# Optimization experiments

Measured on AMD Instinct MI355X. Metric: run time of the kernel, lower is better.

## Reference

```python
import jax, jax.numpy as jnp
import numpy as np

D_MODEL = 1024
N_HEADS = 16
HEAD_DIM = D_MODEL // N_HEADS
SCALE = HEAD_DIM ** -0.5
MASK_FILL = -10000.0


def setup_inputs() -> dict:
    key = jax.random.key(0)
    ks = jax.random.split(key, 12)
    B, L, D = 2, 2048, D_MODEL
    inv = 1.0 / np.sqrt(D)
    inp = {
        "query": jax.random.normal(ks[0], (B, L, D), jnp.float32),
        "key": jax.random.normal(ks[1], (B, L, D), jnp.float32),
        "value": jax.random.normal(ks[2], (B, L, D), jnp.float32),
        "Wq": jax.random.normal(ks[3], (D, D), jnp.float32) * inv,
        "bq": jnp.zeros((D,), jnp.float32),
        "Wk": jax.random.normal(ks[4], (D, D), jnp.float32) * inv,
        "bk": jnp.zeros((D,), jnp.float32),
        "Wv": jax.random.normal(ks[5], (D, D), jnp.float32) * inv,
        "bv": jnp.zeros((D,), jnp.float32),
        "Wo": jax.random.normal(ks[6], (D, D), jnp.float32) * inv,
        "bo": jnp.zeros((D,), jnp.float32),
        "valid_mask": jax.random.randint(ks[7], (B, L), 0, 2).astype(jnp.bool_),
    }
    return inp


def reference(query, key, value, Wq, bq, Wk, bk, Wv, bv, Wo, bo, valid_mask):
    B, Lq, D = query.shape
    Lk = key.shape[1]
    H, HD = N_HEADS, HEAD_DIM
    # torch.nn.Linear: y = x @ W.T + b
    Q = (query @ Wq.T + bq).reshape(B, Lq, H, HD).transpose(0, 2, 1, 3)  # [B,H,Lq,HD]
    K = (key @ Wk.T + bk).reshape(B, Lk, H, HD).transpose(0, 2, 1, 3)    # [B,H,Lk,HD]
    V = (value @ Wv.T + bv).reshape(B, Lk, H, HD).transpose(0, 2, 1, 3)  # [B,H,Lk,HD]
    scores = jnp.einsum("bhqd,bhkd->bhqk", Q, K) * SCALE
    scores = jnp.where(valid_mask[:, None, None, :], scores, MASK_FILL)
    weights = jax.nn.softmax(scores, axis=-1)  # dropout is identity at inference
    out = jnp.einsum("bhqk,bhkd->bhqd", weights, V)
    out = out.transpose(0, 2, 1, 3).reshape(B, Lq, D)
    out = out @ Wo.T + bo
    # zero rows of fully-invalid batches
    gate = jnp.any(valid_mask, axis=1).astype(out.dtype)[:, None, None]
    return out * gate
```

## Files before the change

### kernel.cpp

```cpp
#include <hip/hip_runtime.h>
#include <hip/hip_bf16.h>

typedef __hip_bfloat16 bf16;
typedef __attribute__((ext_vector_type(8))) short s8v;
typedef __attribute__((ext_vector_type(4))) float f4v;

#define LOG2E 1.44269504088896340736f
#define CSCALE (0.125f * LOG2E)
#define MASK_B2 (-14426.950408889634f)

#define BB 2
#define LL 2048
#define DD 1024
#define HH 16
#define HD 64
#define MTOT 4096
#define PER_T 4194304

struct alignas(8) B4 { bf16 v[4]; };

__device__ __forceinline__ void async_cp16(const bf16* g, bf16* l) {
    __builtin_amdgcn_global_load_lds(
        (const __attribute__((address_space(1))) void*)g,
        (__attribute__((address_space(3))) void*)l, 16, 0, 0);
}

struct CvtArgs {
    const float* src[7];
    bf16* dst[7];
    int n[7];
};

__global__ __launch_bounds__(256) void cvt_kernel(CvtArgs args) {
    const int which = blockIdx.y;
    const float* __restrict__ src = args.src[which];
    bf16* __restrict__ dst = args.dst[which];
    const int n4 = args.n[which] >> 2;
    const int stride = gridDim.x * 256;
    for (int i = blockIdx.x * 256 + threadIdx.x; i < n4; i += stride) {
        const float4 f = ((const float4*)src)[i];
        B4 o;
        o.v[0] = __float2bfloat16(f.x);
        o.v[1] = __float2bfloat16(f.y);
        o.v[2] = __float2bfloat16(f.z);
        o.v[3] = __float2bfloat16(f.w);
        ((B4*)dst)[i] = o;
    }
}

struct QkvArgs {
    const bf16* A[3];
    const bf16* W[3];
    const float* bias[3];
    bf16* out[3];
};

template <int SWAP>
__device__ __forceinline__ void gemm_body(const bf16* __restrict__ A,
                                          const bf16* __restrict__ W,
                                          const float* __restrict__ bias,
                                          bf16* __restrict__ out_bf,
                                          char* smem) {
    bf16* sA = (bf16*)smem;
    bf16* sB = (bf16*)(smem + 128 * 64 * 2);
    bf16* sE = (bf16*)smem;

    const int lane = threadIdx.x & 63;
    const int w = threadIdx.x >> 6;
    const int lr = lane & 15;
    const int quad = lane >> 4;
    const int wr = w >> 1, wc = w & 1;
    const int rbase = blockIdx.x * 128;
    const int cbase = blockIdx.y * 128;
    const int dma_r = lane >> 3;
    const int dma_cc = ((lane & 7) ^ dma_r) * 8;

    f4v acc[4][4] = {};
    for (int kt = 0; kt < DD / 64; kt++) {
        const int k0 = kt * 64;
        __syncthreads();
#pragma unroll
        for (int t = 0; t < 4; t++) {
            const int g = w * 4 + t;
            async_cp16(A + (size_t)(rbase + g * 8 + dma_r) * DD + k0 + dma_cc,
                       &sA[g * 512]);
            async_cp16(W + (size_t)(cbase + g * 8 + dma_r) * DD + k0 + dma_cc,
                       &sB[g * 512]);
        }
        __syncthreads();
#pragma unroll
        for (int s = 0; s < 2; s++) {
            s8v a[4], b[4];
#pragma unroll
            for (int i = 0; i < 4; i++) {
                const int row = wr * 64 + i * 16 + lr;
                a[i] = *(const s8v*)&sA[row * 64 + (((s * 4 + quad) ^ (row & 7)) * 8)];
            }
#pragma unroll
            for (int j = 0; j < 4; j++) {
                const int row = wc * 64 + j * 16 + lr;
                b[j] = *(const s8v*)&sB[row * 64 + (((s * 4 + quad) ^ (row & 7)) * 8)];
            }
#pragma unroll
            for (int i = 0; i < 4; i++)
#pragma unroll
                for (int j = 0; j < 4; j++)
                    acc[i][j] = SWAP
                        ? __builtin_amdgcn_mfma_f32_16x16x32_bf16(b[j], a[i], acc[i][j], 0, 0, 0)
                        : __builtin_amdgcn_mfma_f32_16x16x32_bf16(a[i], b[j], acc[i][j], 0, 0, 0);
        }
    }
    __syncthreads();

    if (SWAP) {
#pragma unroll
        for (int j = 0; j < 4; j++) {
            const int n_loc = wc * 64 + j * 16 + quad * 4;
            const f4v bv = *(const f4v*)&bias[cbase + n_loc];
#pragma unroll
            for (int i = 0; i < 4; i++) {
                const int m_loc = wr * 64 + i * 16 + lr;
                B4 pk;
                pk.v[0] = __float2bfloat16(acc[i][j][0] + bv[0]);
                pk.v[1] = __float2bfloat16(acc[i][j][1] + bv[1]);
                pk.v[2] = __float2bfloat16(acc[i][j][2] + bv[2]);
                pk.v[3] = __float2bfloat16(acc[i][j][3] + bv[3]);
                *(B4*)&sE[m_loc * 136 + n_loc] = pk;
            }
        }
        __syncthreads();
        const int tid = threadIdx.x;
        const int mr_ = tid >> 4;
        const int n0 = (tid & 15) * 8;
#pragma unroll
        for (int ro = 0; ro < 8; ro++) {
            const int m_loc = ro * 16 + mr_;
            const s8v vv = *(const s8v*)&sE[m_loc * 136 + n0];
            const int m = rbase + m_loc;
            const int n = cbase + n0;
            const int b_ = m >> 11, l = m & (LL - 1);
            const int h = n >> 6, hd = n & 63;
            *(s8v*)&out_bf[(((size_t)(b_ * HH + h)) * LL + l) * HD + hd] = vv;
        }
    } else {
#pragma unroll
        for (int j = 0; j < 4; j++) {
            const int n_loc = wc * 64 + j * 16 + lr;
            const float bv = bias[cbase + n_loc];
#pragma unroll
            for (int i = 0; i < 4; i++) {
                const int m0 = wr * 64 + i * 16 + quad * 4;
                B4 pk;
                pk.v[0] = __float2bfloat16(acc[i][j][0] + bv);
                pk.v[1] = __float2bfloat16(acc[i][j][1] + bv);
                pk.v[2] = __float2bfloat16(acc[i][j][2] + bv);
                pk.v[3] = __float2bfloat16(acc[i][j][3] + bv);
                *(B4*)&sE[n_loc * 136 + m0] = pk;
            }
        }
        __syncthreads();
        const int tid = threadIdx.x;
#pragma unroll
        for (int ro = 0; ro < 8; ro++) {
            const int n_loc = ro * 16 + (tid >> 4);
            const int m0 = (tid & 15) * 8;
            const s8v vv = *(const s8v*)&sE[n_loc * 136 + m0];
            const int n = cbase + n_loc;
            const int m = rbase + m0;
            const int b_ = m >> 11, l = m & (LL - 1);
            const int h = n >> 6, hd = n & 63;
            *(s8v*)&out_bf[(((size_t)(b_ * HH + h)) * HD + hd) * LL + l] = vv;
        }
    }
}

__global__ __launch_bounds__(256) void gemm128(QkvArgs qa) {
    __shared__ __align__(16) char smem[128 * 136 * 2];
    const int which = blockIdx.z;
    if (which != 2)
        gemm_body<1>(qa.A[which], qa.W[which], qa.bias[which], qa.out[which], smem);
    else
        gemm_body<0>(qa.A[2], qa.W[2], qa.bias[2], qa.out[2], smem);
}

__global__ __launch_bounds__(256) void oproj64(const bf16* __restrict__ A,
                                               const bf16* __restrict__ W,
                                               const float* __restrict__ bias,
                                               float* __restrict__ out_f,
                                               const int* __restrict__ mask) {
    __shared__ bf16 sA[64 * 64];
    __shared__ bf16 sB[128 * 64];
    __shared__ int sgate;

    const int lane = threadIdx.x & 63;
    const int w = threadIdx.x >> 6;
    const int lr = lane & 15;
    const int quad = lane >> 4;
    const int wr = w >> 1, wc = w & 1;
    const int rbase = blockIdx.x * 64;
    const int cbase = blockIdx.y * 128;
    const int dma_r = lane >> 3;
    const int dma_cc = ((lane & 7) ^ dma_r) * 8;

    if (threadIdx.x == 0) sgate = 0;
    __syncthreads();
    const int b_g = rbase >> 11;
    int any = 0;
    for (int i = threadIdx.x; i < LL; i += 256) any |= mask[b_g * LL + i];
    if (any) sgate = 1;

    f4v acc[2][4] = {};
    for (int kt = 0; kt < DD / 64; kt++) {
        const int k0 = kt * 64;
        __syncthreads();
#pragma unroll
        for (int t = 0; t < 2; t++) {
            const int g = w * 2 + t;
            async_cp16(A + (size_t)(rbase + g * 8 + dma_r) * DD + k0 + dma_cc,
                       &sA[g * 512]);
        }
#pragma unroll
        for (int t = 0; t < 4; t++) {
            const int g = w * 4 + t;
            async_cp16(W + (size_t)(cbase + g * 8 + dma_r) * DD + k0 + dma_cc,
                       &sB[g * 512]);
        }
        __syncthreads();
#pragma unroll
        for (int s = 0; s < 2; s++) {
            s8v a[2], b[4];
#pragma unroll
            for (int i = 0; i < 2; i++) {
                const int row = wr * 32 + i * 16 + lr;
                a[i] = *(const s8v*)&sA[row * 64 + (((s * 4 + quad) ^ (row & 7)) * 8)];
            }
#pragma unroll
            for (int j = 0; j < 4; j++) {
                const int row = wc * 64 + j * 16 + lr;
                b[j] = *(const s8v*)&sB[row * 64 + (((s * 4 + quad) ^ (row & 7)) * 8)];
            }
#pragma unroll
            for (int i = 0; i < 2; i++)
#pragma unroll
                for (int j = 0; j < 4; j++)
                    acc[i][j] = __builtin_amdgcn_mfma_f32_16x16x32_bf16(b[j], a[i], acc[i][j], 0, 0, 0);
        }
    }

    const float gatef = sgate ? 1.0f : 0.0f;
#pragma unroll
    for (int j = 0; j < 4; j++) {
        const int n = cbase + wc * 64 + j * 16 + quad * 4;
        const f4v bv = *(const f4v*)&bias[n];
#pragma unroll
        for (int i = 0; i < 2; i++) {
            const int m = rbase + wr * 32 + i * 16 + lr;
            float4 o;
            o.x = (acc[i][j][0] + bv[0]) * gatef;
            o.y = (acc[i][j][1] + bv[1]) * gatef;
            o.z = (acc[i][j][2] + bv[2]) * gatef;
            o.w = (acc[i][j][3] + bv[3]) * gatef;
            *(float4*)&out_f[(size_t)m * DD + n] = o;
        }
    }
}

__global__ __launch_bounds__(512) void attn_kernel(const bf16* __restrict__ Q,
                                                   const bf16* __restrict__ K,
                                                   const bf16* __restrict__ Vt,
                                                   const int* __restrict__ mask,
                                                   bf16* __restrict__ Aout) {
    __shared__ bf16 sK[2][64 * 64];
    __shared__ bf16 sV[2][64 * 64];
    __shared__ float sBias[LL];

    const int lane = threadIdx.x & 63;
    const int w = threadIdx.x >> 6;
    const int lr = lane & 15;
    const int quad = lane >> 4;

    const int bid = blockIdx.x;
    const int qb = bid & 15;
    const int h = (bid >> 4) & 15;
    const int b = bid >> 8;

    const size_t head_off = ((size_t)(b * HH + h)) * LL * HD;
    const bf16* Qh = Q + head_off;
    const bf16* Kh = K + head_off;
    const bf16* Vh = Vt + head_off;
    const int q0 = qb * 128 + w * 16;

    const int dma_r = lane >> 3;
    const int dma_cv = ((lane & 7) ^ dma_r) * 8;
    const int dma_ck = ((lane & 7) ^ ((dma_r & 3) | ((w & 1) << 2))) * 8;

    {
        const int* mb = mask + b * LL;
        for (int i = threadIdx.x; i < LL; i += 512)
            sBias[i] = mb[i] ? 0.0f : MASK_B2;
        async_cp16(Kh + (size_t)(w * 8 + dma_r) * HD + dma_ck, &sK[0][w * 512]);
        async_cp16(Vh + (size_t)(w * 8 + dma_r) * LL + dma_cv, &sV[0][w * 512]);
    }
    __syncthreads();

    const s8v aq0 = *(const s8v*)(Qh + (size_t)(q0 + lr) * HD + quad * 8);
    const s8v aq1 = *(const s8v*)(Qh + (size_t)(q0 + lr) * HD + 32 + quad * 8);

    f4v O[4] = {};
    float lacc = 0.0f;

    const int swk = (lr & 3) | (((lr >> 2) & 1) << 2);
    const int swv = lr & 7;
    const int krow0 = 8 * (lr >> 2) + (lr & 3);

    for (int kt = 0; kt < LL / 64; kt++) {
        const int kbase = kt * 64;
        const bf16* kb = &sK[kt & 1][0];
        const bf16* vb = &sV[kt & 1][0];

        if (kt < LL / 64 - 1) {
            const int nb = (kt + 1) & 1;
            async_cp16(Kh + (size_t)(kbase + 64 + w * 8 + dma_r) * HD + dma_ck,
                       &sK[nb][w * 512]);
            async_cp16(Vh + (size_t)(w * 8 + dma_r) * LL + kbase + 64 + dma_cv,
                       &sV[nb][w * 512]);
        }

        f4v T[4];
        __builtin_amdgcn_s_setprio(1);
#pragma unroll
        for (int j = 0; j < 4; j++) {
            const int row = krow0 + 32 * (j >> 1) + 4 * (j & 1);
            const s8v kb0 = *(const s8v*)&kb[row * 64 + ((quad ^ swk) * 8)];
            const s8v kb1 = *(const s8v*)&kb[row * 64 + (((quad + 4) ^ swk) * 8)];
            f4v t = {};
            t = __builtin_amdgcn_mfma_f32_16x16x32_bf16(kb0, aq0, t, 0, 0, 0);
            T[j] = __builtin_amdgcn_mfma_f32_16x16x32_bf16(kb1, aq1, t, 0, 0, 0);
        }
        __builtin_amdgcn_s_setprio(0);

        s8v v0[4], v1[4];
#pragma unroll
        for (int dt = 0; dt < 4; dt++) {
            const int vrow = dt * 16 + lr;
            v0[dt] = *(const s8v*)&vb[vrow * 64 + ((quad ^ swv) * 8)];
            v1[dt] = *(const s8v*)&vb[vrow * 64 + (((quad + 4) ^ swv) * 8)];
        }

        union { s8v v; bf16 e[8]; } p0, p1;
#pragma unroll
        for (int j = 0; j < 4; j++) {
            const f4v bj = *(const f4v*)&sBias[kbase + 32 * (j >> 1) + 8 * quad + 4 * (j & 1)];
#pragma unroll
            for (int r = 0; r < 4; r++) {
                const float e = exp2f(T[j][r] * CSCALE + bj[r]);
                T[j][r] = e;
                lacc += e;
            }
        }
#pragma unroll
        for (int r = 0; r < 4; r++) {
            p0.e[r]     = __float2bfloat16(T[0][r]);
            p0.e[r + 4] = __float2bfloat16(T[1][r]);
            p1.e[r]     = __float2bfloat16(T[2][r]);
            p1.e[r + 4] = __float2bfloat16(T[3][r]);
        }

        __builtin_amdgcn_s_setprio(1);
#pragma unroll
        for (int dt = 0; dt < 4; dt++) {
            O[dt] = __builtin_amdgcn_mfma_f32_16x16x32_bf16(v0[dt], p0.v, O[dt], 0, 0, 0);
            O[dt] = __builtin_amdgcn_mfma_f32_16x16x32_bf16(v1[dt], p1.v, O[dt], 0, 0, 0);
        }
        __builtin_amdgcn_s_setprio(0);

        __syncthreads();
    }

    float lt = lacc;
    lt += __shfl_xor(lt, 16);
    lt += __shfl_xor(lt, 32);
    const float linv = (lt > 0.0f) ? (1.0f / lt) : 0.0f;

#pragma unroll
    for (int dt = 0; dt < 4; dt++) {
        B4 o;
#pragma unroll
        for (int r = 0; r < 4; r++) o.v[r] = __float2bfloat16(O[dt][r] * linv);
        *(B4*)&Aout[((size_t)(b * LL + q0 + lr)) * DD + h * HD + dt * 16 + quad * 4] = o;
    }
}

extern "C" void kernel_launch(void* const* d_in, const int* in_sizes, int n_in,
                              void* d_out, int out_size, void* d_ws, size_t ws_size,
                              hipStream_t stream) {
    const float* query = (const float*)d_in[0];
    const float* key   = (const float*)d_in[1];
    const float* value = (const float*)d_in[2];
    const float* Wq = (const float*)d_in[3];
    const float* bq = (const float*)d_in[4];
    const float* Wk = (const float*)d_in[5];
    const float* bk = (const float*)d_in[6];
    const float* Wv = (const float*)d_in[7];
    const float* bv = (const float*)d_in[8];
    const float* Wo = (const float*)d_in[9];
    const float* bo = (const float*)d_in[10];
    const int* mask = (const int*)d_in[11];

    bf16* base = (bf16*)d_ws;
    bf16* qx = base;
    bf16* kx = qx + PER_T;
    bf16* vx = kx + PER_T;
    bf16* wq = vx + PER_T;
    bf16* wk = wq + DD * DD;
    bf16* wv = wk + DD * DD;
    bf16* wo = wv + DD * DD;
    bf16* Qs = wo + DD * DD;
    bf16* Ks = Qs + PER_T;
    bf16* Vst = Ks + PER_T;
    bf16* aws = Vst + PER_T;

    CvtArgs ca;
    ca.src[0] = query; ca.dst[0] = qx; ca.n[0] = PER_T;
    ca.src[1] = key;   ca.dst[1] = kx; ca.n[1] = PER_T;
    ca.src[2] = value; ca.dst[2] = vx; ca.n[2] = PER_T;
    ca.src[3] = Wq;    ca.dst[3] = wq; ca.n[3] = DD * DD;
    ca.src[4] = Wk;    ca.dst[4] = wk; ca.n[4] = DD * DD;
    ca.src[5] = Wv;    ca.dst[5] = wv; ca.n[5] = DD * DD;
    ca.src[6] = Wo;    ca.dst[6] = wo; ca.n[6] = DD * DD;
    cvt_kernel<<<dim3(1024, 7), 256, 0, stream>>>(ca);

    QkvArgs qa;
    qa.A[0] = qx; qa.W[0] = wq; qa.bias[0] = bq; qa.out[0] = Qs;
    qa.A[1] = kx; qa.W[1] = wk; qa.bias[1] = bk; qa.out[1] = Ks;
    qa.A[2] = vx; qa.W[2] = wv; qa.bias[2] = bv; qa.out[2] = Vst;

    gemm128<<<dim3(MTOT / 128, DD / 128, 3), 256, 0, stream>>>(qa);

    attn_kernel<<<BB * HH * (LL / 128), 512, 0, stream>>>(Qs, Ks, Vst, mask, aws);

    oproj64<<<dim3(MTOT / 64, DD / 128), 256, 0, stream>>>(
        aws, wo, bo, (float*)d_out, mask);
}
```

Measured before the change: 239.4 us.

## Fuse fp32-to-bf16 activation conversion into QKV GEMM operand loads

The separate conversion pass over query/key/value is removed. The QKV GEMM now streams fp32 activations straight into LDS with an XOR swizzle and converts them to bf16 at fragment-load time. This drops a full read/write pass of roughly 48MB of activations plus the bf16 re-read. The cost is double-size A tiles in LDS, which may cut occupancy, extra conversion ALU work in the inner loop, and re-conversion of each A tile by every column block.

```diff
diff --git a/kernel.cpp b/kernel.cpp
--- a/kernel.cpp
+++ b/kernel.cpp
@@ -19,16 +19,16 @@
 
 struct alignas(8) B4 { bf16 v[4]; };
 
-__device__ __forceinline__ void async_cp16(const bf16* g, bf16* l) {
+__device__ __forceinline__ void async_cp16(const void* g, void* l) {
     __builtin_amdgcn_global_load_lds(
         (const __attribute__((address_space(1))) void*)g,
         (__attribute__((address_space(3))) void*)l, 16, 0, 0);
 }
 
 struct CvtArgs {
-    const float* src[7];
-    bf16* dst[7];
-    int n[7];
+    const float* src[4];
+    bf16* dst[4];
+    int n[4];
 };
 
 __global__ __launch_bounds__(256) void cvt_kernel(CvtArgs args) {
@@ -49,20 +49,20 @@
 }
 
 struct QkvArgs {
-    const bf16* A[3];
+    const float* A[3];
     const bf16* W[3];
     const float* bias[3];
     bf16* out[3];
 };
 
 template <int SWAP>
-__device__ __forceinline__ void gemm_body(const bf16* __restrict__ A,
+__device__ __forceinline__ void gemm_body(const float* __restrict__ Af,
                                           const bf16* __restrict__ W,
                                           const float* __restrict__ bias,
                                           bf16* __restrict__ out_bf,
                                           char* smem) {
-    bf16* sA = (bf16*)smem;
-    bf16* sB = (bf16*)(smem + 128 * 64 * 2);
+    float* sAf = (float*)smem;
+    bf16* sB = (bf16*)(smem + 128 * 64 * 4);
     bf16* sE = (bf16*)smem;
 
     const int lane = threadIdx.x & 63;
@@ -82,10 +82,17 @@
 #pragma unroll
         for (int t = 0; t < 4; t++) {
             const int g = w * 4 + t;
-            async_cp16(A + (size_t)(rbase + g * 8 + dma_r) * DD + k0 + dma_cc,
-                       &sA[g * 512]);
             async_cp16(W + (size_t)(cbase + g * 8 + dma_r) * DD + k0 + dma_cc,
                        &sB[g * 512]);
+#pragma unroll
+            for (int c = 0; c < 2; c++) {
+                const int row_in_g = c * 4 + (lane >> 4);
+                const int swz = (8 * (g & 1) + row_in_g) & 15;
+                const int src_chunk = (lane & 15) ^ swz;
+                async_cp16(Af + (size_t)(rbase + g * 8 + row_in_g) * DD + k0 +
+                               src_chunk * 4,
+                           &sAf[g * 512 + c * 256]);
+            }
         }
         __syncthreads();
 #pragma unroll
@@ -94,7 +101,15 @@
 #pragma unroll
             for (int i = 0; i < 4; i++) {
                 const int row = wr * 64 + i * 16 + lr;
-                a[i] = *(const s8v*)&sA[row * 64 + (((s * 4 + quad) ^ (row & 7)) * 8)];
+                const int C = s * 8 + quad * 2;
+                const f4v fa0 = *(const f4v*)&sAf[row * 64 + ((C ^ lr) * 4)];
+                const f4v fa1 = *(const f4v*)&sAf[row * 64 + (((C + 1) ^ lr) * 4)];
+                union { s8v v; __hip_bfloat162 h[4]; } av;
+                av.h[0] = __float22bfloat162_rn(make_float2(fa0[0], fa0[1]));
+                av.h[1] = __float22bfloat162_rn(make_float2(fa0[2], fa0[3]));
+                av.h[2] = __float22bfloat162_rn(make_float2(fa1[0], fa1[1]));
+                av.h[3] = __float22bfloat162_rn(make_float2(fa1[2], fa1[3]));
+                a[i] = av.v;
             }
 #pragma unroll
             for (int j = 0; j < 4; j++) {
@@ -175,7 +190,7 @@
 }
 
 __global__ __launch_bounds__(256) void gemm128(QkvArgs qa) {
-    __shared__ __align__(16) char smem[128 * 136 * 2];
+    __shared__ __align__(16) char smem[128 * 64 * 4 + 128 * 64 * 2];
     const int which = blockIdx.z;
     if (which != 2)
         gemm_body<1>(qa.A[which], qa.W[which], qa.bias[which], qa.out[which], smem);
@@ -408,10 +423,7 @@
     const int* mask = (const int*)d_in[11];
 
     bf16* base = (bf16*)d_ws;
-    bf16* qx = base;
-    bf16* kx = qx + PER_T;
-    bf16* vx = kx + PER_T;
-    bf16* wq = vx + PER_T;
+    bf16* wq = base;
     bf16* wk = wq + DD * DD;
     bf16* wv = wk + DD * DD;
     bf16* wo = wv + DD * DD;
@@ -421,19 +433,16 @@
     bf16* aws = Vst + PER_T;
 
     CvtArgs ca;
-    ca.src[0] = query; ca.dst[0] = qx; ca.n[0] = PER_T;
-    ca.src[1] = key;   ca.dst[1] = kx; ca.n[1] = PER_T;
-    ca.src[2] = value; ca.dst[2] = vx; ca.n[2] = PER_T;
-    ca.src[3] = Wq;    ca.dst[3] = wq; ca.n[3] = DD * DD;
-    ca.src[4] = Wk;    ca.dst[4] = wk; ca.n[4] = DD * DD;
-    ca.src[5] = Wv;    ca.dst[5] = wv; ca.n[5] = DD * DD;
-    ca.src[6] = Wo;    ca.dst[6] = wo; ca.n[6] = DD * DD;
-    cvt_kernel<<<dim3(1024, 7), 256, 0, stream>>>(ca);
+    ca.src[0] = Wq; ca.dst[0] = wq; ca.n[0] = DD * DD;
+    ca.src[1] = Wk; ca.dst[1] = wk; ca.n[1] = DD * DD;
+    ca.src[2] = Wv; ca.dst[2] = wv; ca.n[2] = DD * DD;
+    ca.src[3] = Wo; ca.dst[3] = wo; ca.n[3] = DD * DD;
+    cvt_kernel<<<dim3(256, 4), 256, 0, stream>>>(ca);
 
     QkvArgs qa;
-    qa.A[0] = qx; qa.W[0] = wq; qa.bias[0] = bq; qa.out[0] = Qs;
-    qa.A[1] = kx; qa.W[1] = wk; qa.bias[1] = bk; qa.out[1] = Ks;
-    qa.A[2] = vx; qa.W[2] = wv; qa.bias[2] = bv; qa.out[2] = Vst;
+    qa.A[0] = query; qa.W[0] = wq; qa.bias[0] = bq; qa.out[0] = Qs;
+    qa.A[1] = key;   qa.W[1] = wk; qa.bias[1] = bk; qa.out[1] = Ks;
+    qa.A[2] = value; qa.W[2] = wv; qa.bias[2] = bv; qa.out[2] = Vst;
 
     gemm128<<<dim3(MTOT / 128, DD / 128, 3), 256, 0, stream>>>(qa);
 
```

Result: slower. 251.9 us (+5.2%).
